# Performance work log

Measured on AMD Instinct MI355X. Metric: run time of the kernel, lower is better.

The kernel has to match this reference:

```python
import jax, jax.numpy as jnp
import numpy as np

N_NODES = 100000
N_EDGES = 1600000
IN_DIM, HID_DIM, OUT_DIM = 128, 64, 32


def gcn_conv(x, edge_index, W, b, n_nodes):
    """PyG GCNConv: add self-loops, symmetric deg^-1/2 normalization,
    linear transform, gather->scatter-sum aggregation, then bias."""
    loops = jnp.arange(n_nodes, dtype=edge_index.dtype)
    src = jnp.concatenate([edge_index[0], loops])  # [E+N]
    dst = jnp.concatenate([edge_index[1], loops])  # [E+N]
    # degree over targets (includes self-loops)
    deg = jax.ops.segment_sum(jnp.ones_like(dst, dtype=x.dtype), dst,
                              num_segments=n_nodes)
    dinv = jnp.where(deg > 0, jax.lax.rsqrt(deg), 0.0)
    norm = dinv[src] * dinv[dst]                   # [E+N]
    h = x @ W                                      # [N, F_out]
    msg = h[src] * norm[:, None]                   # gather + scale
    out = jax.ops.segment_sum(msg, dst, num_segments=n_nodes)
    return out + b


def setup_inputs() -> dict:
    key = jax.random.key(0)
    k1, k2, k3, k4 = jax.random.split(key, 4)
    x = jax.random.normal(k1, (N_NODES, IN_DIM), dtype=jnp.float32)
    edge_index = jax.random.randint(k2, (2, N_EDGES), 0, N_NODES,
                                    dtype=jnp.int64)
    # Glorot-ish init for weights, zero bias (PyG default: glorot + zeros)
    W1 = jax.random.normal(k3, (IN_DIM, HID_DIM), dtype=jnp.float32) * (1.0 / np.sqrt(IN_DIM))
    b1 = jnp.zeros((HID_DIM,), dtype=jnp.float32)
    W2 = jax.random.normal(k4, (HID_DIM, OUT_DIM), dtype=jnp.float32) * (1.0 / np.sqrt(HID_DIM))
    b2 = jnp.zeros((OUT_DIM,), dtype=jnp.float32)
    return {"x": x, "edge_index": edge_index, "W1": W1, "b1": b1,
            "W2": W2, "b2": b2}


def reference(x, edge_index, W1, b1, W2, b2):
    n = x.shape[0]
    h = jax.nn.relu(gcn_conv(x, edge_index, W1, b1, n))
    return gcn_conv(h, edge_index, W2, b2, n)
```

## Files before the change

kernel.cpp:

```cpp
#include <hip/hip_runtime.h>


#define BLK 256
#define BLKC 1024
#define EPT 8
#define CITER 18
#define BSHIFT 10
#define NPB 1024
#define SLOTB 18432
#define NBMAX 128

typedef unsigned int uint_t;
typedef unsigned short ushort_t;
typedef __attribute__((ext_vector_type(2))) float v2f;
typedef __attribute__((ext_vector_type(8))) short bf16x8;
typedef __attribute__((ext_vector_type(4))) float f32x4;

__device__ __forceinline__ uint_t f2bf(float x) {
    union { float f; uint_t u; } un; un.f = x;
    uint_t u = un.u;
    return (u + 0x7fffu + ((u >> 16) & 1u)) >> 16;
}

__device__ __forceinline__ void pkadd(v2f& a0, v2f& a1, v2f& a2, v2f& a3, uint4 v) {
    v2f p;
    p.x = __uint_as_float(v.x << 16); p.y = __uint_as_float(v.x & 0xffff0000u); a0 += p;
    p.x = __uint_as_float(v.y << 16); p.y = __uint_as_float(v.y & 0xffff0000u); a1 += p;
    p.x = __uint_as_float(v.z << 16); p.y = __uint_as_float(v.z & 0xffff0000u); a2 += p;
    p.x = __uint_as_float(v.w << 16); p.y = __uint_as_float(v.w & 0xffff0000u); a3 += p;
}

__device__ __forceinline__ bool detect64(const int* __restrict__ idx) {
    int z = 0;
#pragma unroll
    for (int i = 1; i < 32; i += 2) z |= idx[i];
    return z == 0;
}

__global__ void k_part(const int* __restrict__ idx, int* __restrict__ bcursor,
                       int* __restrict__ edge_part, int E, int nbuck) {
    __shared__ int h[NBMAX];
    __shared__ int rb[NBMAX];
    bool is64 = detect64(idx);
    int t = threadIdx.x, blk = blockIdx.x;
    for (int i = t; i < nbuck; i += BLK) h[i] = 0;
    __syncthreads();
    int base = blk * (BLK * EPT) + t;
    int dst[EPT], src[EPT], rk[EPT];
#pragma unroll
    for (int k = 0; k < EPT; ++k) {
        int e = base + k * BLK;
        if (e < E) {
            if (is64) {
                uint2 dv = ((const uint2*)idx)[(size_t)E + e];
                uint2 sv = ((const uint2*)idx)[e];
                dst[k] = (int)dv.x;
                src[k] = (int)sv.x;
            } else {
                dst[k] = idx[E + e];
                src[k] = idx[e];
            }
            rk[k] = atomicAdd(&h[dst[k] >> BSHIFT], 1);
        } else {
            dst[k] = -1;
        }
    }
    __syncthreads();
    for (int i = t; i < nbuck; i += BLK) {
        int c = h[i];
        rb[i] = c ? atomicAdd(&bcursor[i], c) : 0;
    }
    __syncthreads();
#pragma unroll
    for (int k = 0; k < EPT; ++k) {
        if (dst[k] >= 0) {
            int b = dst[k] >> BSHIFT;
            edge_part[(size_t)b * SLOTB + rb[b] + rk[k]] =
                src[k] | ((dst[k] & (NPB - 1)) << 17);
        }
    }
}

__global__ __launch_bounds__(BLKC) void k_csr(
        const int* __restrict__ edge_part, const int* __restrict__ bcursor,
        int* __restrict__ row_ptr, int* __restrict__ deg, float* __restrict__ dinv,
        int* __restrict__ csr_src, int N, int nbuck) {
    __shared__ int cnt[NPB];
    __shared__ int off[NPB];
    int b = blockIdx.x, t = threadIdx.x;
    int node0 = b << BSHIFT;
    int nn = min(NPB, N - node0);
    int m = bcursor[b];
    size_t ebase = (size_t)b * SLOTB;
    cnt[t] = 0;
    __syncthreads();
    int pp[CITER], rr[CITER];
#pragma unroll
    for (int it = 0; it < CITER; ++it) {
        int e = t + it * BLKC;
        if (e < m) {
            int p = edge_part[ebase + e];
            pp[it] = p;
            rr[it] = atomicAdd(&cnt[((unsigned)p) >> 17], 1);
        }
    }
    __syncthreads();
    off[t] = cnt[t];
    __syncthreads();
    for (int st = 1; st < BLKC; st <<= 1) {
        int v = (t >= st) ? off[t - st] : 0;
        __syncthreads();
        off[t] += v;
        __syncthreads();
    }
    int excl = off[t] - cnt[t];
    off[t] = excl;
    if (t < nn) {
        row_ptr[node0 + t] = (int)(ebase + excl);
        deg[node0 + t] = cnt[t];
        dinv[node0 + t] = rsqrtf((float)(cnt[t] + 1));
    }
    __syncthreads();
#pragma unroll
    for (int it = 0; it < CITER; ++it) {
        int e = t + it * BLKC;
        if (e < m) {
            int p = pp[it];
            int dlo = ((unsigned)p) >> 17;
            csr_src[ebase + off[dlo] + rr[it]] = p & 0x1FFFF;
        }
    }
}

__global__ __launch_bounds__(256) void k_gemm1(
        const float* __restrict__ x, const float* __restrict__ W1,
        const float* __restrict__ dinv, ushort_t* __restrict__ hs1, int N) {
    __shared__ ushort_t xb[64][136];
    __shared__ ushort_t wb[64][136];
    int t = threadIdx.x;
    int rbase = blockIdx.x * 64;
    for (int i = t; i < 2048; i += BLK) {
        int k = i >> 4, n4 = i & 15;
        float4 w = ((const float4*)W1)[i];
        wb[4 * n4 + 0][k] = (ushort_t)f2bf(w.x);
        wb[4 * n4 + 1][k] = (ushort_t)f2bf(w.y);
        wb[4 * n4 + 2][k] = (ushort_t)f2bf(w.z);
        wb[4 * n4 + 3][k] = (ushort_t)f2bf(w.w);
    }
    for (int i = t; i < 2048; i += BLK) {
        int r = i >> 5, c4 = i & 31;
        int rr = rbase + r; if (rr >= N) rr = N - 1;
        float4 v = ((const float4*)x)[(size_t)rr * 32 + c4];
        uint2 p;
        p.x = f2bf(v.x) | (f2bf(v.y) << 16);
        p.y = f2bf(v.z) | (f2bf(v.w) << 16);
        *(uint2*)&xb[r][4 * c4] = p;
    }
    __syncthreads();
    int w = t >> 6, l = t & 63;
    int lane16 = l & 15, quad = l >> 4;
    int mrow = 16 * w + lane16;
    f32x4 acc0 = {0.f, 0.f, 0.f, 0.f}, acc1 = {0.f, 0.f, 0.f, 0.f};
    f32x4 acc2 = {0.f, 0.f, 0.f, 0.f}, acc3 = {0.f, 0.f, 0.f, 0.f};
#pragma unroll
    for (int kk = 0; kk < 4; ++kk) {
        int k0 = kk * 32 + quad * 8;
        bf16x8 a  = *(const bf16x8*)&xb[mrow][k0];
        bf16x8 b0 = *(const bf16x8*)&wb[lane16][k0];
        bf16x8 b1 = *(const bf16x8*)&wb[lane16 + 16][k0];
        bf16x8 b2 = *(const bf16x8*)&wb[lane16 + 32][k0];
        bf16x8 b3 = *(const bf16x8*)&wb[lane16 + 48][k0];
        acc0 = __builtin_amdgcn_mfma_f32_16x16x32_bf16(a, b0, acc0, 0, 0, 0);
        acc1 = __builtin_amdgcn_mfma_f32_16x16x32_bf16(a, b1, acc1, 0, 0, 0);
        acc2 = __builtin_amdgcn_mfma_f32_16x16x32_bf16(a, b2, acc2, 0, 0, 0);
        acc3 = __builtin_amdgcn_mfma_f32_16x16x32_bf16(a, b3, acc3, 0, 0, 0);
    }
    __syncthreads();
    int orow = 16 * w + quad * 4;
    float d0 = dinv[min(rbase + orow + 0, N - 1)];
    float d1 = dinv[min(rbase + orow + 1, N - 1)];
    float d2 = dinv[min(rbase + orow + 2, N - 1)];
    float d3 = dinv[min(rbase + orow + 3, N - 1)];
    xb[orow + 0][lane16]      = (ushort_t)f2bf(acc0.x * d0);
    xb[orow + 1][lane16]      = (ushort_t)f2bf(acc0.y * d1);
    xb[orow + 2][lane16]      = (ushort_t)f2bf(acc0.z * d2);
    xb[orow + 3][lane16]      = (ushort_t)f2bf(acc0.w * d3);
    xb[orow + 0][lane16 + 16] = (ushort_t)f2bf(acc1.x * d0);
    xb[orow + 1][lane16 + 16] = (ushort_t)f2bf(acc1.y * d1);
    xb[orow + 2][lane16 + 16] = (ushort_t)f2bf(acc1.z * d2);
    xb[orow + 3][lane16 + 16] = (ushort_t)f2bf(acc1.w * d3);
    xb[orow + 0][lane16 + 32] = (ushort_t)f2bf(acc2.x * d0);
    xb[orow + 1][lane16 + 32] = (ushort_t)f2bf(acc2.y * d1);
    xb[orow + 2][lane16 + 32] = (ushort_t)f2bf(acc2.z * d2);
    xb[orow + 3][lane16 + 32] = (ushort_t)f2bf(acc2.w * d3);
    xb[orow + 0][lane16 + 48] = (ushort_t)f2bf(acc3.x * d0);
    xb[orow + 1][lane16 + 48] = (ushort_t)f2bf(acc3.y * d1);
    xb[orow + 2][lane16 + 48] = (ushort_t)f2bf(acc3.z * d2);
    xb[orow + 3][lane16 + 48] = (ushort_t)f2bf(acc3.w * d3);
    __syncthreads();
    for (int i = t; i < 512; i += BLK) {
        int r = i >> 3, c8 = i & 7;
        int rr = rbase + r;
        if (rr < N) {
            uint4 v = *(const uint4*)&xb[r][8 * c8];
            *(uint4*)&hs1[(size_t)rr * 64 + 8 * c8] = v;
        }
    }
}

__global__ void k_agg1(const uint_t* __restrict__ hs1, const int* __restrict__ row_ptr,
                       const int* __restrict__ deg, const int* __restrict__ csr_src,
                       const float* __restrict__ dinv, const float* __restrict__ b1,
                       ushort_t* __restrict__ a1b, int N) {
    int lane = threadIdx.x & 63;
    int g = lane >> 3;
    int c = lane & 7;
    int wavebase = ((blockIdx.x * blockDim.x + threadIdx.x) >> 6) * 8;
    int node = wavebase + g;
    bool alive = node < N;
    int nodeC = alive ? node : N - 1;
    const uint4* H = (const uint4*)hs1;
    float dn = dinv[nodeC];
    int beg = row_ptr[nodeC];
    int tot = alive ? deg[nodeC] : 0;
    uint4 selfv = H[(size_t)nodeC * 8 + c];
    int gbase = lane & 0x38;
    int wtot = tot;
    wtot = max(wtot, __shfl_xor(wtot, 8, 64));
    wtot = max(wtot, __shfl_xor(wtot, 16, 64));
    wtot = max(wtot, __shfl_xor(wtot, 32, 64));
    int nch = (wtot + 7) >> 3;
    v2f a0 = {0.f, 0.f}, a1_ = {0.f, 0.f}, a2 = {0.f, 0.f}, a3 = {0.f, 0.f};
    uint4 vA[8], vB[8];
    auto ISSUE = [&](uint4 (&vv)[8], int i) {
        int base = 8 * i;
        int jal = (base + c < tot) ? csr_src[beg + base + c] : 0;
#pragma unroll
        for (int e = 0; e < 8; ++e) {
            int j = __shfl(jal, gbase + e, 64);
            if (base + e < tot) vv[e] = H[(size_t)j * 8 + c];
        }
    };
    auto CONSUME = [&](uint4 (&vv)[8], int i) {
        int base = 8 * i;
#pragma unroll
        for (int e = 0; e < 8; ++e)
            if (base + e < tot) pkadd(a0, a1_, a2, a3, vv[e]);
    };
    if (nch > 0) {
        ISSUE(vA, 0);
        int i = 1;
        for (; i + 1 < nch; i += 2) {
            ISSUE(vB, i);     CONSUME(vA, i - 1);
            ISSUE(vA, i + 1); CONSUME(vB, i);
        }
        if (i < nch) { ISSUE(vB, i); CONSUME(vA, i - 1); CONSUME(vB, i); }
        else          CONSUME(vA, i - 1);
    }
    pkadd(a0, a1_, a2, a3, selfv);
    if (alive) {
        const float4* B = (const float4*)b1;
        float4 bv0 = B[2 * c], bv1 = B[2 * c + 1];
        float o0 = fmaxf(fmaf(a0.x, dn, bv0.x), 0.f);
        float o1 = fmaxf(fmaf(a0.y, dn, bv0.y), 0.f);
        float o2 = fmaxf(fmaf(a1_.x, dn, bv0.z), 0.f);
        float o3 = fmaxf(fmaf(a1_.y, dn, bv0.w), 0.f);
        float o4 = fmaxf(fmaf(a2.x, dn, bv1.x), 0.f);
        float o5 = fmaxf(fmaf(a2.y, dn, bv1.y), 0.f);
        float o6 = fmaxf(fmaf(a3.x, dn, bv1.z), 0.f);
        float o7 = fmaxf(fmaf(a3.y, dn, bv1.w), 0.f);
        uint4 o;
        o.x = f2bf(o0) | (f2bf(o1) << 16);
        o.y = f2bf(o2) | (f2bf(o3) << 16);
        o.z = f2bf(o4) | (f2bf(o5) << 16);
        o.w = f2bf(o6) | (f2bf(o7) << 16);
        ((uint4*)a1b)[(size_t)node * 8 + c] = o;
    }
}

__global__ __launch_bounds__(256) void k_gemm2(
        const ushort_t* __restrict__ a1b, const float* __restrict__ W2,
        const float* __restrict__ dinv, ushort_t* __restrict__ hs2, int N) {
    __shared__ ushort_t ab[64][72];
    __shared__ ushort_t wb[32][72];
    int t = threadIdx.x;
    int rbase = blockIdx.x * 64;
    for (int i = t; i < 512; i += BLK) {
        int k = i >> 3, n4 = i & 7;
        float4 w = ((const float4*)W2)[i];
        wb[4 * n4 + 0][k] = (ushort_t)f2bf(w.x);
        wb[4 * n4 + 1][k] = (ushort_t)f2bf(w.y);
        wb[4 * n4 + 2][k] = (ushort_t)f2bf(w.z);
        wb[4 * n4 + 3][k] = (ushort_t)f2bf(w.w);
    }
    for (int i = t; i < 512; i += BLK) {
        int r = i >> 3, c8 = i & 7;
        int rr = rbase + r; if (rr >= N) rr = N - 1;
        uint4 v = ((const uint4*)a1b)[(size_t)rr * 8 + c8];
        *(uint4*)&ab[r][8 * c8] = v;
    }
    __syncthreads();
    int w = t >> 6, l = t & 63;
    int lane16 = l & 15, quad = l >> 4;
    int mrow = 16 * w + lane16;
    f32x4 acc0 = {0.f, 0.f, 0.f, 0.f}, acc1 = {0.f, 0.f, 0.f, 0.f};
#pragma unroll
    for (int kk = 0; kk < 2; ++kk) {
        int k0 = kk * 32 + quad * 8;
        bf16x8 a  = *(const bf16x8*)&ab[mrow][k0];
        bf16x8 b0 = *(const bf16x8*)&wb[lane16][k0];
        bf16x8 b1 = *(const bf16x8*)&wb[lane16 + 16][k0];
        acc0 = __builtin_amdgcn_mfma_f32_16x16x32_bf16(a, b0, acc0, 0, 0, 0);
        acc1 = __builtin_amdgcn_mfma_f32_16x16x32_bf16(a, b1, acc1, 0, 0, 0);
    }
    __syncthreads();
    int orow = 16 * w + quad * 4;
    float d0 = dinv[min(rbase + orow + 0, N - 1)];
    float d1 = dinv[min(rbase + orow + 1, N - 1)];
    float d2 = dinv[min(rbase + orow + 2, N - 1)];
    float d3 = dinv[min(rbase + orow + 3, N - 1)];
    ab[orow + 0][lane16]      = (ushort_t)f2bf(acc0.x * d0);
    ab[orow + 1][lane16]      = (ushort_t)f2bf(acc0.y * d1);
    ab[orow + 2][lane16]      = (ushort_t)f2bf(acc0.z * d2);
    ab[orow + 3][lane16]      = (ushort_t)f2bf(acc0.w * d3);
    ab[orow + 0][lane16 + 16] = (ushort_t)f2bf(acc1.x * d0);
    ab[orow + 1][lane16 + 16] = (ushort_t)f2bf(acc1.y * d1);
    ab[orow + 2][lane16 + 16] = (ushort_t)f2bf(acc1.z * d2);
    ab[orow + 3][lane16 + 16] = (ushort_t)f2bf(acc1.w * d3);
    __syncthreads();
    for (int i = t; i < 256; i += BLK) {
        int r = i >> 2, c4 = i & 3;
        int rr = rbase + r;
        if (rr < N) {
            uint4 v = *(const uint4*)&ab[r][8 * c4];
            *(uint4*)&hs2[(size_t)rr * 32 + 8 * c4] = v;
        }
    }
}

__global__ void k_agg2(const uint_t* __restrict__ hs2, const int* __restrict__ row_ptr,
                       const int* __restrict__ deg, const int* __restrict__ csr_src,
                       const float* __restrict__ dinv, const float* __restrict__ b2,
                       float* __restrict__ out, int N) {
    int lane = threadIdx.x & 63;
    int g = lane >> 2;
    int c = lane & 3;
    int wavebase = ((blockIdx.x * blockDim.x + threadIdx.x) >> 6) * 16;
    int node = wavebase + g;
    bool alive = node < N;
    int nodeC = alive ? node : N - 1;
    const uint4* H = (const uint4*)hs2;
    float dn = dinv[nodeC];
    int beg = row_ptr[nodeC];
    int tot = alive ? deg[nodeC] : 0;
    uint4 selfv = H[(size_t)nodeC * 4 + c];
    int gbase = lane & 0x3C;
    int wtot = tot;
    wtot = max(wtot, __shfl_xor(wtot, 4, 64));
    wtot = max(wtot, __shfl_xor(wtot, 8, 64));
    wtot = max(wtot, __shfl_xor(wtot, 16, 64));
    wtot = max(wtot, __shfl_xor(wtot, 32, 64));
    int nch = (wtot + 3) >> 2;
    v2f a0 = {0.f, 0.f}, a1_ = {0.f, 0.f}, a2 = {0.f, 0.f}, a3 = {0.f, 0.f};
    uint4 vA[4], vB[4];
    auto ISSUE = [&](uint4 (&vv)[4], int i) {
        int base = 4 * i;
        int jal = (base + c < tot) ? csr_src[beg + base + c] : 0;
#pragma unroll
        for (int e = 0; e < 4; ++e) {
            int j = __shfl(jal, gbase + e, 64);
            if (base + e < tot) vv[e] = H[(size_t)j * 4 + c];
        }
    };
    auto CONSUME = [&](uint4 (&vv)[4], int i) {
        int base = 4 * i;
#pragma unroll
        for (int e = 0; e < 4; ++e)
            if (base + e < tot) pkadd(a0, a1_, a2, a3, vv[e]);
    };
    if (nch > 0) {
        ISSUE(vA, 0);
        int i = 1;
        for (; i + 1 < nch; i += 2) {
            ISSUE(vB, i);     CONSUME(vA, i - 1);
            ISSUE(vA, i + 1); CONSUME(vB, i);
        }
        if (i < nch) { ISSUE(vB, i); CONSUME(vA, i - 1); CONSUME(vB, i); }
        else          CONSUME(vA, i - 1);
    }
    pkadd(a0, a1_, a2, a3, selfv);
    if (alive) {
        const float4* B = (const float4*)b2;
        float4 bv0 = B[2 * c], bv1 = B[2 * c + 1];
        float4 o0, o1;
        o0.x = fmaf(a0.x, dn, bv0.x);
        o0.y = fmaf(a0.y, dn, bv0.y);
        o0.z = fmaf(a1_.x, dn, bv0.z);
        o0.w = fmaf(a1_.y, dn, bv0.w);
        o1.x = fmaf(a2.x, dn, bv1.x);
        o1.y = fmaf(a2.y, dn, bv1.y);
        o1.z = fmaf(a3.x, dn, bv1.z);
        o1.w = fmaf(a3.y, dn, bv1.w);
        float4* O = (float4*)out;
        O[(size_t)node * 8 + 2 * c] = o0;
        O[(size_t)node * 8 + 2 * c + 1] = o1;
    }
}

extern "C" void kernel_launch(void* const* d_in, const int* in_sizes, int n_in,
                              void* d_out, int out_size, void* d_ws, size_t ws_size,
                              hipStream_t stream) {
    const float* x  = (const float*)d_in[0];
    const int*   idx = (const int*)d_in[1];
    const float* W1 = (const float*)d_in[2];
    const float* b1 = (const float*)d_in[3];
    const float* W2 = (const float*)d_in[4];
    const float* b2 = (const float*)d_in[5];
    float* out = (float*)d_out;

    const int N = in_sizes[0] / 128;
    const int E = in_sizes[1] / 2;
    const int nbuck = (N + NPB - 1) >> BSHIFT;
    const int PB = (E + BLK * EPT - 1) / (BLK * EPT);

    char* ws = (char*)d_ws;
    size_t off = 0;
    auto alloc = [&](size_t bytes) -> char* {
        char* p = ws + off;
        off = (off + bytes + 255) & ~(size_t)255;
        return p;
    };
    float* dinv     = (float*)alloc((size_t)N * 4);
    int*   row_ptr  = (int*)alloc((size_t)N * 4);
    int*   deg      = (int*)alloc((size_t)N * 4);
    int*   bcursor  = (int*)alloc((size_t)nbuck * 4);
    int*   csr_src  = (int*)alloc((size_t)nbuck * SLOTB * 4);
    size_t ep_bytes = (size_t)nbuck * SLOTB * 4;
    size_t h1_bytes = (size_t)N * 64 * 2;
    int*   edge_part = (int*)alloc(ep_bytes > h1_bytes ? ep_bytes : h1_bytes);
    ushort_t* a1b   = (ushort_t*)alloc((size_t)N * 64 * 2);
    ushort_t* hs1   = (ushort_t*)edge_part;
    ushort_t* hs2   = hs1;

    hipMemsetAsync(bcursor, 0, (size_t)nbuck * 4, stream);
    k_part<<<PB, BLK, 0, stream>>>(idx, bcursor, edge_part, E, nbuck);
    k_csr<<<nbuck, BLKC, 0, stream>>>(edge_part, bcursor, row_ptr, deg, dinv,
                                      csr_src, N, nbuck);
    k_gemm1<<<(N + 63) / 64, BLK, 0, stream>>>(x, W1, dinv, hs1, N);
    k_agg1<<<(N * 8 + BLK - 1) / BLK, BLK, 0, stream>>>(
        (const uint_t*)hs1, row_ptr, deg, csr_src, dinv, b1, a1b, N);
    k_gemm2<<<(N + 63) / 64, BLK, 0, stream>>>(a1b, W2, dinv, hs2, N);
    k_agg2<<<(N * 4 + BLK - 1) / BLK, BLK, 0, stream>>>(
        (const uint_t*)hs2, row_ptr, deg, csr_src, dinv, b2, out, N);
}
```

Measured before the change: 220.4 us.

## Pre-transpose bf16 weights once, use hardware bf16 pack, and wave-shuffle scan

An extra block in the partition kernel converts W1 and W2 to transposed bf16 once into a small workspace buffer. The GEMM kernels then copy it with vector loads instead of each block converting and transposing the weights into LDS. All software round-to-nearest bf16 conversions are replaced with the packed v_cvt_pk_bf16_f32 instruction. The CSR kernel's barrier-heavy Hillis-Steele LDS scan becomes a two-level wave-shuffle scan. Together these cut redundant per-block weight work, ALU conversion cost and barrier count.

```diff
diff --git a/kernel.cpp b/kernel.cpp
--- a/kernel.cpp
+++ b/kernel.cpp
@@ -16,10 +16,10 @@
 typedef __attribute__((ext_vector_type(8))) short bf16x8;
 typedef __attribute__((ext_vector_type(4))) float f32x4;
 
-__device__ __forceinline__ uint_t f2bf(float x) {
-    union { float f; uint_t u; } un; un.f = x;
-    uint_t u = un.u;
-    return (u + 0x7fffu + ((u >> 16) & 1u)) >> 16;
+__device__ __forceinline__ uint_t pkbf(float lo, float hi) {
+    uint_t r;
+    asm("v_cvt_pk_bf16_f32 %0, %1, %2" : "=v"(r) : "v"(lo), "v"(hi));
+    return r;
 }
 
 __device__ __forceinline__ void pkadd(v2f& a0, v2f& a1, v2f& a2, v2f& a3, uint4 v) {
@@ -38,7 +38,37 @@
 }
 
 __global__ void k_part(const int* __restrict__ idx, int* __restrict__ bcursor,
-                       int* __restrict__ edge_part, int E, int nbuck) {
+                       int* __restrict__ edge_part,
+                       const float* __restrict__ W1, const float* __restrict__ W2,
+                       ushort_t* __restrict__ wt, int E, int nbuck, int PB) {
+    if (blockIdx.x == PB) {
+        int t = threadIdx.x;
+        int n = t >> 2, q = t & 3;
+        uint_t buf[16];
+#pragma unroll
+        for (int i = 0; i < 16; ++i) {
+            float a = W1[(size_t)(32 * q + 2 * i) * 64 + n];
+            float b = W1[(size_t)(32 * q + 2 * i + 1) * 64 + n];
+            buf[i] = pkbf(a, b);
+        }
+#pragma unroll
+        for (int i = 0; i < 4; ++i)
+            ((uint4*)wt)[(size_t)n * 16 + q * 4 + i] = *(uint4*)&buf[4 * i];
+        if (t < 128) {
+            int n2 = t >> 2, q2 = t & 3;
+            uint_t b2[8];
+#pragma unroll
+            for (int i = 0; i < 8; ++i) {
+                float a = W2[(size_t)(16 * q2 + 2 * i) * 32 + n2];
+                float b = W2[(size_t)(16 * q2 + 2 * i + 1) * 32 + n2];
+                b2[i] = pkbf(a, b);
+            }
+#pragma unroll
+            for (int i = 0; i < 2; ++i)
+                ((uint4*)(wt + 8192))[(size_t)n2 * 8 + q2 * 2 + i] = *(uint4*)&b2[4 * i];
+        }
+        return;
+    }
     __shared__ int h[NBMAX];
     __shared__ int rb[NBMAX];
     bool is64 = detect64(idx);
@@ -87,6 +117,7 @@
         int* __restrict__ csr_src, int N, int nbuck) {
     __shared__ int cnt[NPB];
     __shared__ int off[NPB];
+    __shared__ int wsum[16];
     int b = blockIdx.x, t = threadIdx.x;
     int node0 = b << BSHIFT;
     int nn = min(NPB, N - node0);
@@ -105,20 +136,31 @@
         }
     }
     __syncthreads();
-    off[t] = cnt[t];
-    __syncthreads();
-    for (int st = 1; st < BLKC; st <<= 1) {
-        int v = (t >= st) ? off[t - st] : 0;
-        __syncthreads();
-        off[t] += v;
-        __syncthreads();
-    }
-    int excl = off[t] - cnt[t];
+    int cown = cnt[t];
+    int xi = cown;
+#pragma unroll
+    for (int d = 1; d < 64; d <<= 1) {
+        int y = __shfl_up(xi, d, 64);
+        if ((t & 63) >= d) xi += y;
+    }
+    if ((t & 63) == 63) wsum[t >> 6] = xi;
+    __syncthreads();
+    if (t < 16) {
+        int wv = wsum[t];
+#pragma unroll
+        for (int d = 1; d < 16; d <<= 1) {
+            int y = __shfl_up(wv, d, 64);
+            if (t >= d) wv += y;
+        }
+        wsum[t] = wv;
+    }
+    __syncthreads();
+    int excl = xi - cown + ((t >= 64) ? wsum[(t >> 6) - 1] : 0);
     off[t] = excl;
     if (t < nn) {
         row_ptr[node0 + t] = (int)(ebase + excl);
-        deg[node0 + t] = cnt[t];
-        dinv[node0 + t] = rsqrtf((float)(cnt[t] + 1));
+        deg[node0 + t] = cown;
+        dinv[node0 + t] = rsqrtf((float)(cown + 1));
     }
     __syncthreads();
 #pragma unroll
@@ -133,27 +175,24 @@
 }
 
 __global__ __launch_bounds__(256) void k_gemm1(
-        const float* __restrict__ x, const float* __restrict__ W1,
+        const float* __restrict__ x, const ushort_t* __restrict__ wt,
         const float* __restrict__ dinv, ushort_t* __restrict__ hs1, int N) {
     __shared__ ushort_t xb[64][136];
     __shared__ ushort_t wb[64][136];
     int t = threadIdx.x;
     int rbase = blockIdx.x * 64;
-    for (int i = t; i < 2048; i += BLK) {
-        int k = i >> 4, n4 = i & 15;
-        float4 w = ((const float4*)W1)[i];
-        wb[4 * n4 + 0][k] = (ushort_t)f2bf(w.x);
-        wb[4 * n4 + 1][k] = (ushort_t)f2bf(w.y);
-        wb[4 * n4 + 2][k] = (ushort_t)f2bf(w.z);
-        wb[4 * n4 + 3][k] = (ushort_t)f2bf(w.w);
+    for (int i = t; i < 1024; i += BLK) {
+        int n = i >> 4, q = i & 15;
+        uint4 v = ((const uint4*)wt)[i];
+        *(uint4*)&wb[n][8 * q] = v;
     }
     for (int i = t; i < 2048; i += BLK) {
         int r = i >> 5, c4 = i & 31;
         int rr = rbase + r; if (rr >= N) rr = N - 1;
         float4 v = ((const float4*)x)[(size_t)rr * 32 + c4];
         uint2 p;
-        p.x = f2bf(v.x) | (f2bf(v.y) << 16);
-        p.y = f2bf(v.z) | (f2bf(v.w) << 16);
+        p.x = pkbf(v.x, v.y);
+        p.y = pkbf(v.z, v.w);
         *(uint2*)&xb[r][4 * c4] = p;
     }
     __syncthreads();
@@ -181,22 +220,23 @@
     float d1 = dinv[min(rbase + orow + 1, N - 1)];
     float d2 = dinv[min(rbase + orow + 2, N - 1)];
     float d3 = dinv[min(rbase + orow + 3, N - 1)];
-    xb[orow + 0][lane16]      = (ushort_t)f2bf(acc0.x * d0);
-    xb[orow + 1][lane16]      = (ushort_t)f2bf(acc0.y * d1);
-    xb[orow + 2][lane16]      = (ushort_t)f2bf(acc0.z * d2);
-    xb[orow + 3][lane16]      = (ushort_t)f2bf(acc0.w * d3);
-    xb[orow + 0][lane16 + 16] = (ushort_t)f2bf(acc1.x * d0);
-    xb[orow + 1][lane16 + 16] = (ushort_t)f2bf(acc1.y * d1);
-    xb[orow + 2][lane16 + 16] = (ushort_t)f2bf(acc1.z * d2);
-    xb[orow + 3][lane16 + 16] = (ushort_t)f2bf(acc1.w * d3);
-    xb[orow + 0][lane16 + 32] = (ushort_t)f2bf(acc2.x * d0);
-    xb[orow + 1][lane16 + 32] = (ushort_t)f2bf(acc2.y * d1);
-    xb[orow + 2][lane16 + 32] = (ushort_t)f2bf(acc2.z * d2);
-    xb[orow + 3][lane16 + 32] = (ushort_t)f2bf(acc2.w * d3);
-    xb[orow + 0][lane16 + 48] = (ushort_t)f2bf(acc3.x * d0);
-    xb[orow + 1][lane16 + 48] = (ushort_t)f2bf(acc3.y * d1);
-    xb[orow + 2][lane16 + 48] = (ushort_t)f2bf(acc3.z * d2);
-    xb[orow + 3][lane16 + 48] = (ushort_t)f2bf(acc3.w * d3);
+    uint_t u;
+    u = pkbf(acc0.x * d0, acc0.y * d1);
+    xb[orow + 0][lane16] = (ushort_t)u;  xb[orow + 1][lane16] = (ushort_t)(u >> 16);
+    u = pkbf(acc0.z * d2, acc0.w * d3);
+    xb[orow + 2][lane16] = (ushort_t)u;  xb[orow + 3][lane16] = (ushort_t)(u >> 16);
+    u = pkbf(acc1.x * d0, acc1.y * d1);
+    xb[orow + 0][lane16 + 16] = (ushort_t)u;  xb[orow + 1][lane16 + 16] = (ushort_t)(u >> 16);
+    u = pkbf(acc1.z * d2, acc1.w * d3);
+    xb[orow + 2][lane16 + 16] = (ushort_t)u;  xb[orow + 3][lane16 + 16] = (ushort_t)(u >> 16);
+    u = pkbf(acc2.x * d0, acc2.y * d1);
+    xb[orow + 0][lane16 + 32] = (ushort_t)u;  xb[orow + 1][lane16 + 32] = (ushort_t)(u >> 16);
+    u = pkbf(acc2.z * d2, acc2.w * d3);
+    xb[orow + 2][lane16 + 32] = (ushort_t)u;  xb[orow + 3][lane16 + 32] = (ushort_t)(u >> 16);
+    u = pkbf(acc3.x * d0, acc3.y * d1);
+    xb[orow + 0][lane16 + 48] = (ushort_t)u;  xb[orow + 1][lane16 + 48] = (ushort_t)(u >> 16);
+    u = pkbf(acc3.z * d2, acc3.w * d3);
+    xb[orow + 2][lane16 + 48] = (ushort_t)u;  xb[orow + 3][lane16 + 48] = (ushort_t)(u >> 16);
     __syncthreads();
     for (int i = t; i < 512; i += BLK) {
         int r = i >> 3, c8 = i & 7;
@@ -270,28 +310,25 @@
         float o6 = fmaxf(fmaf(a3.x, dn, bv1.z), 0.f);
         float o7 = fmaxf(fmaf(a3.y, dn, bv1.w), 0.f);
         uint4 o;
-        o.x = f2bf(o0) | (f2bf(o1) << 16);
-        o.y = f2bf(o2) | (f2bf(o3) << 16);
-        o.z = f2bf(o4) | (f2bf(o5) << 16);
-        o.w = f2bf(o6) | (f2bf(o7) << 16);
+        o.x = pkbf(o0, o1);
+        o.y = pkbf(o2, o3);
+        o.z = pkbf(o4, o5);
+        o.w = pkbf(o6, o7);
         ((uint4*)a1b)[(size_t)node * 8 + c] = o;
     }
 }
 
 __global__ __launch_bounds__(256) void k_gemm2(
-        const ushort_t* __restrict__ a1b, const float* __restrict__ W2,
+        const ushort_t* __restrict__ a1b, const ushort_t* __restrict__ wt,
         const float* __restrict__ dinv, ushort_t* __restrict__ hs2, int N) {
     __shared__ ushort_t ab[64][72];
     __shared__ ushort_t wb[32][72];
     int t = threadIdx.x;
     int rbase = blockIdx.x * 64;
-    for (int i = t; i < 512; i += BLK) {
-        int k = i >> 3, n4 = i & 7;
-        float4 w = ((const float4*)W2)[i];
-        wb[4 * n4 + 0][k] = (ushort_t)f2bf(w.x);
-        wb[4 * n4 + 1][k] = (ushort_t)f2bf(w.y);
-        wb[4 * n4 + 2][k] = (ushort_t)f2bf(w.z);
-        wb[4 * n4 + 3][k] = (ushort_t)f2bf(w.w);
+    for (int i = t; i < 256; i += BLK) {
+        int n = i >> 3, q = i & 7;
+        uint4 v = ((const uint4*)(wt + 8192))[i];
+        *(uint4*)&wb[n][8 * q] = v;
     }
     for (int i = t; i < 512; i += BLK) {
         int r = i >> 3, c8 = i & 7;
@@ -319,14 +356,15 @@
     float d1 = dinv[min(rbase + orow + 1, N - 1)];
     float d2 = dinv[min(rbase + orow + 2, N - 1)];
     float d3 = dinv[min(rbase + orow + 3, N - 1)];
-    ab[orow + 0][lane16]      = (ushort_t)f2bf(acc0.x * d0);
-    ab[orow + 1][lane16]      = (ushort_t)f2bf(acc0.y * d1);
-    ab[orow + 2][lane16]      = (ushort_t)f2bf(acc0.z * d2);
-    ab[orow + 3][lane16]      = (ushort_t)f2bf(acc0.w * d3);
-    ab[orow + 0][lane16 + 16] = (ushort_t)f2bf(acc1.x * d0);
-    ab[orow + 1][lane16 + 16] = (ushort_t)f2bf(acc1.y * d1);
-    ab[orow + 2][lane16 + 16] = (ushort_t)f2bf(acc1.z * d2);
-    ab[orow + 3][lane16 + 16] = (ushort_t)f2bf(acc1.w * d3);
+    uint_t u;
+    u = pkbf(acc0.x * d0, acc0.y * d1);
+    ab[orow + 0][lane16] = (ushort_t)u;  ab[orow + 1][lane16] = (ushort_t)(u >> 16);
+    u = pkbf(acc0.z * d2, acc0.w * d3);
+    ab[orow + 2][lane16] = (ushort_t)u;  ab[orow + 3][lane16] = (ushort_t)(u >> 16);
+    u = pkbf(acc1.x * d0, acc1.y * d1);
+    ab[orow + 0][lane16 + 16] = (ushort_t)u;  ab[orow + 1][lane16 + 16] = (ushort_t)(u >> 16);
+    u = pkbf(acc1.z * d2, acc1.w * d3);
+    ab[orow + 2][lane16 + 16] = (ushort_t)u;  ab[orow + 3][lane16 + 16] = (ushort_t)(u >> 16);
     __syncthreads();
     for (int i = t; i < 256; i += BLK) {
         int r = i >> 2, c4 = i & 3;
@@ -434,6 +472,7 @@
     int*   row_ptr  = (int*)alloc((size_t)N * 4);
     int*   deg      = (int*)alloc((size_t)N * 4);
     int*   bcursor  = (int*)alloc((size_t)nbuck * 4);
+    ushort_t* wt    = (ushort_t*)alloc((size_t)(8192 + 2048) * 2);
     int*   csr_src  = (int*)alloc((size_t)nbuck * SLOTB * 4);
     size_t ep_bytes = (size_t)nbuck * SLOTB * 4;
     size_t h1_bytes = (size_t)N * 64 * 2;
@@ -443,13 +482,14 @@
     ushort_t* hs2   = hs1;
 
     hipMemsetAsync(bcursor, 0, (size_t)nbuck * 4, stream);
-    k_part<<<PB, BLK, 0, stream>>>(idx, bcursor, edge_part, E, nbuck);
+    k_part<<<PB + 1, BLK, 0, stream>>>(idx, bcursor, edge_part, W1, W2, wt,
+                                       E, nbuck, PB);
     k_csr<<<nbuck, BLKC, 0, stream>>>(edge_part, bcursor, row_ptr, deg, dinv,
                                       csr_src, N, nbuck);
-    k_gemm1<<<(N + 63) / 64, BLK, 0, stream>>>(x, W1, dinv, hs1, N);
+    k_gemm1<<<(N + 63) / 64, BLK, 0, stream>>>(x, wt, dinv, hs1, N);
     k_agg1<<<(N * 8 + BLK - 1) / BLK, BLK, 0, stream>>>(
         (const uint_t*)hs1, row_ptr, deg, csr_src, dinv, b1, a1b, N);
-    k_gemm2<<<(N + 63) / 64, BLK, 0, stream>>>(a1b, W2, dinv, hs2, N);
+    k_gemm2<<<(N + 63) / 64, BLK, 0, stream>>>(a1b, wt, dinv, hs2, N);
     k_agg2<<<(N * 4 + BLK - 1) / BLK, BLK, 0, stream>>>(
         (const uint_t*)hs2, row_ptr, deg, csr_src, dinv, b2, out, N);
 }
```

Result: faster. 214.3 us (-2.7%).
